# Optimization experiments

Measured on AMD Instinct MI355X. Metric: run time of the kernel, lower is better.

Reference implementation:

```python
import jax, jax.numpy as jnp
import numpy as np

N, E = 50000, 1600000
F_IN, F_EDGE, HID = 128, 16, 64
SLOPE = 0.2
EPS_BN = 1e-5


def setup_inputs() -> dict:
    key = jax.random.key(0)
    ks = jax.random.split(key, 24)
    g = lambda k, shp, s=0.1: (jax.random.normal(k, shp, dtype=jnp.float32) * s)
    inp = {
        'x': jax.random.normal(ks[0], (N, F_IN), dtype=jnp.float32),
        'edge_index': jax.random.randint(ks[1], (2, E), 0, N, dtype=jnp.int64),
        'edge_attr': jax.random.normal(ks[2], (E, F_EDGE), dtype=jnp.float32),
        # conv1: F_IN -> HID, 4 heads, concat
        'W1': g(ks[3], (F_IN, 4 * HID)), 'a1s': g(ks[4], (4, HID)), 'a1d': g(ks[5], (4, HID)), 'b1': jnp.zeros((4 * HID,), jnp.float32),
        # conv2: 4*HID -> HID, 4 heads, concat
        'W2': g(ks[6], (4 * HID, 4 * HID)), 'a2s': g(ks[7], (4, HID)), 'a2d': g(ks[8], (4, HID)), 'b2': jnp.zeros((4 * HID,), jnp.float32),
        # conv3: 4*HID -> HID, 1 head
        'W3': g(ks[9], (4 * HID, HID)), 'a3s': g(ks[10], (1, HID)), 'a3d': g(ks[11], (1, HID)), 'b3': jnp.zeros((HID,), jnp.float32),
        'bn1_g': jnp.ones((4 * HID,), jnp.float32), 'bn1_b': jnp.zeros((4 * HID,), jnp.float32),
        'bn2_g': jnp.ones((4 * HID,), jnp.float32), 'bn2_b': jnp.zeros((4 * HID,), jnp.float32),
        'mlp_W1': g(ks[12], (F_EDGE, HID)), 'mlp_b1': jnp.zeros((HID,), jnp.float32),
        'mlp_W2': g(ks[13], (HID, HID)), 'mlp_b2': jnp.zeros((HID,), jnp.float32),
        'fc_W': g(ks[14], (3 * HID, 1)), 'fc_b': jnp.zeros((1,), jnp.float32),
    }
    return inp


def _gat(x, W, a_s, a_d, b, src, dst, heads, dout):
    n = x.shape[0]
    h = (x @ W).reshape(n, heads, dout)                    # [N,H,D]
    ls = jnp.sum(h * a_s, axis=-1)                         # [N,H]
    ld = jnp.sum(h * a_d, axis=-1)
    logits = jax.nn.leaky_relu(ls[src] + ld[dst], SLOPE)   # [E',H]
    m = jax.ops.segment_max(logits, dst, num_segments=n)
    m = jnp.where(jnp.isfinite(m), m, 0.0)
    p = jnp.exp(logits - m[dst])
    s = jax.ops.segment_sum(p, dst, num_segments=n)
    alpha = p / (s[dst] + 1e-16)                           # segment softmax over in-edges
    out = jax.ops.segment_sum(h[src] * alpha[:, :, None], dst, num_segments=n)
    return out.reshape(n, heads * dout) + b


def _bn(x, g, b):
    mu = jnp.mean(x, axis=0)
    var = jnp.var(x, axis=0)
    return (x - mu) * jax.lax.rsqrt(var + EPS_BN) * g + b


def reference(x, edge_index, edge_attr, W1, a1s, a1d, b1, W2, a2s, a2d, b2,
              W3, a3s, a3d, b3, bn1_g, bn1_b, bn2_g, bn2_b,
              mlp_W1, mlp_b1, mlp_W2, mlp_b2, fc_W, fc_b):
    src0, dst0 = edge_index[0], edge_index[1]
    loop = jnp.arange(x.shape[0], dtype=edge_index.dtype)  # PyG adds self-loops
    src = jnp.concatenate([src0, loop])
    dst = jnp.concatenate([dst0, loop])

    h = _gat(x, W1, a1s, a1d, b1, src, dst, 4, HID)
    h = _bn(jax.nn.elu(h), bn1_g, bn1_b)
    h = _gat(h, W2, a2s, a2d, b2, src, dst, 4, HID)
    h = _bn(jax.nn.elu(h), bn2_g, bn2_b)
    h = _gat(h, W3, a3s, a3d, b3, src, dst, 1, HID)        # [N,HID]

    ef = jax.nn.relu(edge_attr @ mlp_W1 + mlp_b1) @ mlp_W2 + mlp_b2  # [E,HID]
    emb = jnp.concatenate([h[src0], h[dst0], ef], axis=1)  # [E,3*HID]
    return (emb @ fc_W + fc_b).squeeze(-1)
```

## Files before the change

kernel.cpp:

```cpp
#include <hip/hip_runtime.h>
#include <hip/hip_fp16.h>
#include <math.h>


#define FIN 128
#define HID 64
#define BIN_SHIFT 8

typedef _Float16 f16x8 __attribute__((ext_vector_type(8)));
typedef float f32x4 __attribute__((ext_vector_type(4)));

__device__ __forceinline__ unsigned short f2hbits(float f) {
    __half h = __float2half(f);
    return *reinterpret_cast<unsigned short*>(&h);
}
__device__ __forceinline__ float2 hpair(unsigned w) {
    __half2 h = *reinterpret_cast<__half2*>(&w);
    return __half22float2(h);
}

__device__ __forceinline__ unsigned fenc(float f) {
    unsigned b = __float_as_uint(f);
    return (b & 0x80000000u) ? ~b : (b | 0x80000000u);
}
__device__ __forceinline__ float fdec(unsigned k) {
    unsigned b = (k & 0x80000000u) ? (k ^ 0x80000000u) : ~k;
    return __uint_as_float(b);
}


__global__ __launch_bounds__(256) void bincount_kernel(const int* __restrict__ ei,
                                                       int* __restrict__ bincnt,
                                                       int E, int Etot) {
    __shared__ int h[256];
    int t = threadIdx.x;
    h[t] = 0;
    __syncthreads();
    int base = blockIdx.x * 4096;
    #pragma unroll
    for (int i = 0; i < 16; ++i) {
        int e = base + i * 256 + t;
        if (e < Etot) {
            int d = (e < E) ? ei[E + e] : (e - E);
            atomicAdd(&h[d >> BIN_SHIFT], 1);
        }
    }
    __syncthreads();
    if (h[t]) atomicAdd(&bincnt[t], h[t]);
}

__global__ void scanbins_kernel(const int* __restrict__ bincnt, int* __restrict__ binptr,
                                int* __restrict__ bincur, int NB, int Etot) {
    __shared__ int buf[256];
    int t = threadIdx.x;
    int v = (t < NB) ? bincnt[t] : 0;
    buf[t] = v;
    __syncthreads();
    for (int o = 1; o < 256; o <<= 1) {
        int y = (t >= o) ? buf[t - o] : 0;
        __syncthreads();
        buf[t] += y;
        __syncthreads();
    }
    int excl = buf[t] - v;
    if (t < NB) {
        binptr[t] = excl;
        bincur[t] = excl;
    }
    if (t == 0) binptr[NB] = Etot;
}

__global__ __launch_bounds__(256) void binscatter_kernel(const int* __restrict__ ei,
                                                         int* __restrict__ bincur,
                                                         int2* __restrict__ binned,
                                                         int E, int Etot) {
    __shared__ int h[256];
    __shared__ int gb[256];
    int t = threadIdx.x;
    h[t] = 0;
    __syncthreads();
    int base = blockIdx.x * 4096;
    #pragma unroll
    for (int i = 0; i < 16; ++i) {
        int e = base + i * 256 + t;
        if (e < Etot) {
            int d = (e < E) ? ei[E + e] : (e - E);
            atomicAdd(&h[d >> BIN_SHIFT], 1);
        }
    }
    __syncthreads();
    int cnt = h[t];
    if (cnt) gb[t] = atomicAdd(&bincur[t], cnt);
    __syncthreads();
    h[t] = 0;
    __syncthreads();
    #pragma unroll
    for (int i = 0; i < 16; ++i) {
        int e = base + i * 256 + t;
        if (e < Etot) {
            int s, d;
            if (e < E) { s = ei[e]; d = ei[E + e]; }
            else       { s = e - E; d = e - E; }
            int b = d >> BIN_SHIFT;
            int pos = gb[b] + atomicAdd(&h[b], 1);
            binned[pos] = make_int2(s, d);
        }
    }
}

__global__ __launch_bounds__(256) void bincsr_kernel(const int2* __restrict__ binned,
                                                     const int* __restrict__ binptr,
                                                     int* __restrict__ row_ptr,
                                                     int* __restrict__ col,
                                                     int N, int Etot) {
    __shared__ int h[256];
    __shared__ int cur[256];
    __shared__ int wsum[4];
    int b = blockIdx.x;
    int t = threadIdx.x;
    int lo = b << BIN_SHIFT;
    h[t] = 0;
    __syncthreads();
    int ebeg = binptr[b], eend = binptr[b + 1];
    for (int i = ebeg + t; i < eend; i += 256) atomicAdd(&h[binned[i].y - lo], 1);
    __syncthreads();
    int v = h[t];
    int lane = t & 63, w = t >> 6;
    int x = v;
    #pragma unroll
    for (int o = 1; o < 64; o <<= 1) {
        int y = __shfl_up(x, o);
        if (lane >= o) x += y;
    }
    if (lane == 63) wsum[w] = x;
    __syncthreads();
    int off = 0;
    #pragma unroll
    for (int i = 0; i < 4; ++i) off += (i < w) ? wsum[i] : 0;
    int excl = ebeg + off + x - v;
    int node = lo + t;
    if (node < N) row_ptr[node] = excl;
    cur[t] = excl;
    if (b == 0 && t == 0) row_ptr[N] = Etot;
    __syncthreads();
    for (int i = ebeg + t; i < eend; i += 256) {
        int2 sd = binned[i];
        int pos = atomicAdd(&cur[sd.y - lo], 1);
        col[pos] = sd.x;
    }
}


__global__ __launch_bounds__(256) void mfma_gemm_kernel(
    const float* __restrict__ X, const float* __restrict__ W,
    unsigned short* __restrict__ Yh, int Nrows, int K, int M,
    const float* __restrict__ bnsum, const float* __restrict__ bng,
    const float* __restrict__ bnb, float invN,
    const float* __restrict__ as_, const float* __restrict__ ad_,
    float* __restrict__ ls, float* __restrict__ ld,
    unsigned* __restrict__ lsmax_g, int slicedY) {
    __shared__ __align__(16) unsigned short a_lds[128][40];
    __shared__ __align__(16) unsigned short b_lds[64][40];
    __shared__ __align__(16) float scale_l[256];
    __shared__ __align__(16) float shift_l[256];
    __shared__ unsigned lmax_l;
    const int t = threadIdx.x;
    const int row0 = blockIdx.x * 128;
    const int by = blockIdx.y;
    const int c0 = by * 64;
    const int w = t >> 6, lane = t & 63;
    const int quad = lane >> 4, mrow = lane & 15;
    if (t == 0) lmax_l = 0;
    if (bnsum && t < 256) {
        float mu = bnsum[t] * invN;
        float var = bnsum[256 + t] * invN - mu * mu;
        float sc = bng[t] * rsqrtf(var + 1e-5f);
        scale_l[t] = sc;
        shift_l[t] = bnb[t] - mu * sc;
    }
    __syncthreads();
    f32x4 acc[2][4] = {};
    for (int k0 = 0; k0 < K; k0 += 32) {
        #pragma unroll
        for (int i = 0; i < 4; ++i) {
            int f = i * 256 + t;
            int r = f >> 3, kq = f & 7;
            int grow = row0 + r;
            float4 xv = make_float4(0.f, 0.f, 0.f, 0.f);
            if (grow < Nrows) xv = *(const float4*)(X + (size_t)grow * K + k0 + kq * 4);
            if (bnsum) {
                float4 sc = *(const float4*)&scale_l[k0 + kq * 4];
                float4 sh = *(const float4*)&shift_l[k0 + kq * 4];
                xv.x = fmaf(xv.x, sc.x, sh.x);
                xv.y = fmaf(xv.y, sc.y, sh.y);
                xv.z = fmaf(xv.z, sc.z, sh.z);
                xv.w = fmaf(xv.w, sc.w, sh.w);
            }
            ushort4 pk;
            pk.x = f2hbits(xv.x);
            pk.y = f2hbits(xv.y);
            pk.z = f2hbits(xv.z);
            pk.w = f2hbits(xv.w);
            *(ushort4*)&a_lds[r][kq * 4] = pk;
        }
        #pragma unroll
        for (int i = 0; i < 2; ++i) {
            int f = i * 256 + t;
            int kr = f >> 4, cq = f & 15;
            float4 wv = *(const float4*)(W + (size_t)(k0 + kr) * M + c0 + cq * 4);
            b_lds[cq * 4 + 0][kr] = f2hbits(wv.x);
            b_lds[cq * 4 + 1][kr] = f2hbits(wv.y);
            b_lds[cq * 4 + 2][kr] = f2hbits(wv.z);
            b_lds[cq * 4 + 3][kr] = f2hbits(wv.w);
        }
        __syncthreads();
        f16x8 a0 = *(const f16x8*)&a_lds[w * 32 + mrow][quad * 8];
        f16x8 a1 = *(const f16x8*)&a_lds[w * 32 + 16 + mrow][quad * 8];
        #pragma unroll
        for (int c = 0; c < 4; ++c) {
            f16x8 bf = *(const f16x8*)&b_lds[c * 16 + mrow][quad * 8];
            acc[0][c] = __builtin_amdgcn_mfma_f32_16x16x32_f16(a0, bf, acc[0][c], 0, 0, 0);
            acc[1][c] = __builtin_amdgcn_mfma_f32_16x16x32_f16(a1, bf, acc[1][c], 0, 0, 0);
        }
        __syncthreads();
    }
    #pragma unroll
    for (int i = 0; i < 2; ++i) {
        #pragma unroll
        for (int c = 0; c < 4; ++c) {
            #pragma unroll
            for (int r = 0; r < 4; ++r) {
                int grow = row0 + w * 32 + i * 16 + quad * 4 + r;
                if (grow < Nrows) {
                    int ch = c0 + c * 16 + mrow;
                    size_t idx = slicedY
                        ? ((size_t)(ch >> 5) * Nrows + grow) * 32 + (ch & 31)
                        : (size_t)grow * M + ch;
                    Yh[idx] = f2hbits(acc[i][c][r]);
                }
            }
        }
    }
    float asv[4], adv[4];
    #pragma unroll
    for (int c = 0; c < 4; ++c) {
        asv[c] = as_[by * 64 + c * 16 + mrow];
        adv[c] = ad_[by * 64 + c * 16 + mrow];
    }
    float lmax = -3.0e38f;
    #pragma unroll
    for (int i = 0; i < 2; ++i) {
        #pragma unroll
        for (int r = 0; r < 4; ++r) {
            float ps = 0.f, pd = 0.f;
            #pragma unroll
            for (int c = 0; c < 4; ++c) {
                ps = fmaf(acc[i][c][r], asv[c], ps);
                pd = fmaf(acc[i][c][r], adv[c], pd);
            }
            #pragma unroll
            for (int o = 1; o <= 8; o <<= 1) {
                ps += __shfl_xor(ps, o);
                pd += __shfl_xor(pd, o);
            }
            int grow = row0 + w * 32 + i * 16 + quad * 4 + r;
            if (mrow == 0 && grow < Nrows) {
                ls[(size_t)by * Nrows + grow] = ps;
                ld[(size_t)by * Nrows + grow] = pd;
                lmax = fmaxf(lmax, ps);
            }
        }
    }
    if (mrow == 0) atomicMax(&lmax_l, fenc(lmax));
    __syncthreads();
    if (t == 0) atomicMax(&lsmax_g[by], lmax_l);
}


#define ACC8(hv, p)                                              \
    {                                                            \
        float2 fa = hpair((hv).x), fb = hpair((hv).y);           \
        float2 fc = hpair((hv).z), fd = hpair((hv).w);           \
        a0 = fmaf((p), fa.x, a0); a1 = fmaf((p), fa.y, a1);      \
        a2 = fmaf((p), fb.x, a2); a3 = fmaf((p), fb.y, a3);      \
        a4 = fmaf((p), fc.x, a4); a5 = fmaf((p), fc.y, a5);      \
        a6 = fmaf((p), fd.x, a6); a7 = fmaf((p), fd.y, a7);      \
    }

#define COMPUTE_BATCH(l0_, l1_, l2_, l3_, h0_, h1_, h2_, h3_)    \
    {                                                            \
        float g0 = (l0_) + ldn_h; g0 = fmaxf(g0, 0.2f * g0);     \
        float g1 = (l1_) + ldn_h; g1 = fmaxf(g1, 0.2f * g1);     \
        float g2 = (l2_) + ldn_h; g2 = fmaxf(g2, 0.2f * g2);     \
        float g3 = (l3_) + ldn_h; g3 = fmaxf(g3, 0.2f * g3);     \
        float p0 = __expf(g0 - m_h), p1 = __expf(g1 - m_h);      \
        float p2 = __expf(g2 - m_h), p3 = __expf(g3 - m_h);      \
        psum += (p0 + p1) + (p2 + p3);                           \
        ACC8(h0_, p0) ACC8(h1_, p1) ACC8(h2_, p2) ACC8(h3_, p3)  \
    }

__global__ __launch_bounds__(256, 4) void agg_bn_kernel(
    const unsigned short* __restrict__ hb, const float* __restrict__ ls,
    const float* __restrict__ ld, const int* __restrict__ row_ptr,
    const int* __restrict__ col, const float* __restrict__ bias,
    const unsigned* __restrict__ lsmax_g, float* __restrict__ out,
    float* __restrict__ bnsum, int N) {
    __shared__ float redS[4][32];
    __shared__ float redQ[4][32];
    const int t = threadIdx.x;
    const int w = t >> 6, lane = t & 63;
    const int slice = blockIdx.x & 7;
    const int g = lane >> 2;
    const int c4 = lane & 3;
    const int hd = slice >> 1;
    const char* hsl = (const char*)hb + (size_t)slice * (size_t)N * 64u;
    const float* __restrict__ lsp = ls + (size_t)hd * N;
    const float* __restrict__ ldp = ld + (size_t)hd * N;
    const unsigned cb = (unsigned)c4 * 16u;
    const int cbase = slice * 32 + c4 * 8;
    const float lsm = fdec(lsmax_g[hd]);
    const float4 bvA = *(const float4*)(bias + cbase);
    const float4 bvB = *(const float4*)(bias + cbase + 4);
    const int sgid = (int)(blockIdx.x >> 3) * 64 + w * 16 + g;
    const int nsg = (int)(gridDim.x >> 3) * 64;
    float bns0 = 0.f, bns1 = 0.f, bns2 = 0.f, bns3 = 0.f;
    float bns4 = 0.f, bns5 = 0.f, bns6 = 0.f, bns7 = 0.f;
    float bnq0 = 0.f, bnq1 = 0.f, bnq2 = 0.f, bnq3 = 0.f;
    float bnq4 = 0.f, bnq5 = 0.f, bnq6 = 0.f, bnq7 = 0.f;
    for (int n = sgid; n < N; n += nsg) {
        int beg = row_ptr[n], end = row_ptr[n + 1];
        float ldn_h = ldp[n];
        float m_h = fmaxf(0.f, ldn_h + lsm);
        float psum = 0.f;
        float a0 = 0.f, a1 = 0.f, a2 = 0.f, a3 = 0.f;
        float a4 = 0.f, a5 = 0.f, a6 = 0.f, a7 = 0.f;
        int j = beg;
        const bool have = (j + 4 <= end);
        uint4 h0, h1, h2, h3;
        float l0 = 0.f, l1 = 0.f, l2 = 0.f, l3 = 0.f;
        if (have) {
            int s0 = col[j], s1 = col[j + 1], s2 = col[j + 2], s3 = col[j + 3];
            h0 = *(const uint4*)(hsl + ((unsigned)s0 * 64u + cb));
            h1 = *(const uint4*)(hsl + ((unsigned)s1 * 64u + cb));
            h2 = *(const uint4*)(hsl + ((unsigned)s2 * 64u + cb));
            h3 = *(const uint4*)(hsl + ((unsigned)s3 * 64u + cb));
            l0 = lsp[s0]; l1 = lsp[s1]; l2 = lsp[s2]; l3 = lsp[s3];
        }
        for (; j + 8 <= end; j += 4) {
            int n0 = col[j + 4], n1 = col[j + 5], n2 = col[j + 6], n3 = col[j + 7];
            uint4 q0 = *(const uint4*)(hsl + ((unsigned)n0 * 64u + cb));
            uint4 q1 = *(const uint4*)(hsl + ((unsigned)n1 * 64u + cb));
            uint4 q2 = *(const uint4*)(hsl + ((unsigned)n2 * 64u + cb));
            uint4 q3 = *(const uint4*)(hsl + ((unsigned)n3 * 64u + cb));
            float m0 = lsp[n0], m1 = lsp[n1], m2 = lsp[n2], m3 = lsp[n3];
            COMPUTE_BATCH(l0, l1, l2, l3, h0, h1, h2, h3)
            h0 = q0; h1 = q1; h2 = q2; h3 = q3;
            l0 = m0; l1 = m1; l2 = m2; l3 = m3;
        }
        if (have) {
            COMPUTE_BATCH(l0, l1, l2, l3, h0, h1, h2, h3)
            j += 4;
        }
        for (; j < end; ++j) {
            int s = col[j];
            uint4 hv = *(const uint4*)(hsl + ((unsigned)s * 64u + cb));
            float lv = lsp[s];
            float gg = lv + ldn_h; gg = fmaxf(gg, 0.2f * gg);
            float pv = __expf(gg - m_h);
            psum += pv;
            ACC8(hv, pv)
        }
        float inv = 1.f / (psum + 1e-16f);
        float o0 = fmaf(a0, inv, bvA.x);
        float o1 = fmaf(a1, inv, bvA.y);
        float o2 = fmaf(a2, inv, bvA.z);
        float o3 = fmaf(a3, inv, bvA.w);
        float o4 = fmaf(a4, inv, bvB.x);
        float o5 = fmaf(a5, inv, bvB.y);
        float o6 = fmaf(a6, inv, bvB.z);
        float o7 = fmaf(a7, inv, bvB.w);
        o0 = (o0 > 0.f) ? o0 : expm1f(o0);
        o1 = (o1 > 0.f) ? o1 : expm1f(o1);
        o2 = (o2 > 0.f) ? o2 : expm1f(o2);
        o3 = (o3 > 0.f) ? o3 : expm1f(o3);
        o4 = (o4 > 0.f) ? o4 : expm1f(o4);
        o5 = (o5 > 0.f) ? o5 : expm1f(o5);
        o6 = (o6 > 0.f) ? o6 : expm1f(o6);
        o7 = (o7 > 0.f) ? o7 : expm1f(o7);
        float* orow = out + (size_t)n * 256 + cbase;
        *(float4*)orow = make_float4(o0, o1, o2, o3);
        *(float4*)(orow + 4) = make_float4(o4, o5, o6, o7);
        bns0 += o0; bnq0 += o0 * o0;
        bns1 += o1; bnq1 += o1 * o1;
        bns2 += o2; bnq2 += o2 * o2;
        bns3 += o3; bnq3 += o3 * o3;
        bns4 += o4; bnq4 += o4 * o4;
        bns5 += o5; bnq5 += o5 * o5;
        bns6 += o6; bnq6 += o6 * o6;
        bns7 += o7; bnq7 += o7 * o7;
    }
    #pragma unroll
    for (int o = 4; o <= 32; o <<= 1) {
        bns0 += __shfl_xor(bns0, o); bnq0 += __shfl_xor(bnq0, o);
        bns1 += __shfl_xor(bns1, o); bnq1 += __shfl_xor(bnq1, o);
        bns2 += __shfl_xor(bns2, o); bnq2 += __shfl_xor(bnq2, o);
        bns3 += __shfl_xor(bns3, o); bnq3 += __shfl_xor(bnq3, o);
        bns4 += __shfl_xor(bns4, o); bnq4 += __shfl_xor(bnq4, o);
        bns5 += __shfl_xor(bns5, o); bnq5 += __shfl_xor(bnq5, o);
        bns6 += __shfl_xor(bns6, o); bnq6 += __shfl_xor(bnq6, o);
        bns7 += __shfl_xor(bns7, o); bnq7 += __shfl_xor(bnq7, o);
    }
    if (g == 0) {
        redS[w][c4 * 8 + 0] = bns0; redQ[w][c4 * 8 + 0] = bnq0;
        redS[w][c4 * 8 + 1] = bns1; redQ[w][c4 * 8 + 1] = bnq1;
        redS[w][c4 * 8 + 2] = bns2; redQ[w][c4 * 8 + 2] = bnq2;
        redS[w][c4 * 8 + 3] = bns3; redQ[w][c4 * 8 + 3] = bnq3;
        redS[w][c4 * 8 + 4] = bns4; redQ[w][c4 * 8 + 4] = bnq4;
        redS[w][c4 * 8 + 5] = bns5; redQ[w][c4 * 8 + 5] = bnq5;
        redS[w][c4 * 8 + 6] = bns6; redQ[w][c4 * 8 + 6] = bnq6;
        redS[w][c4 * 8 + 7] = bns7; redQ[w][c4 * 8 + 7] = bnq7;
    }
    __syncthreads();
    if (t < 32) {
        float s = redS[0][t] + redS[1][t] + redS[2][t] + redS[3][t];
        float q = redQ[0][t] + redQ[1][t] + redQ[2][t] + redQ[3][t];
        atomicAdd(&bnsum[slice * 32 + t], s);
        atomicAdd(&bnsum[256 + slice * 32 + t], q);
    }
}


__global__ __launch_bounds__(256) void agg3_kernel(
    const unsigned short* __restrict__ hb, const float* __restrict__ ls,
    const float* __restrict__ ld, const int* __restrict__ row_ptr,
    const int* __restrict__ col, const float* __restrict__ bias,
    const float* __restrict__ fcW, float* __restrict__ up, float* __restrict__ vp,
    const unsigned* __restrict__ lsmax_g, int N) {
    int lane = threadIdx.x & 63;
    int n = blockIdx.x * 4 + (threadIdx.x >> 6);
    if (n >= N) return;
    int beg = row_ptr[n], end = row_ptr[n + 1];
    float ldn = ld[n];
    float m_h = fmaxf(0.f, ldn + fdec(lsmax_g[0]));
    int g = lane >> 3;
    int li = lane & 7;
    int c0 = li * 8;
    const char* hbb = (const char*)hb;
    const unsigned cb = (unsigned)c0 * 2u;
    float psum = 0.f;
    float a0 = 0.f, a1 = 0.f, a2 = 0.f, a3 = 0.f;
    float a4 = 0.f, a5 = 0.f, a6 = 0.f, a7 = 0.f;
    for (int j = beg + g; j < end; j += 8) {
        int s = col[j];
        uint4 hv = *(const uint4*)(hbb + ((unsigned)s * 128u + cb));
        float lg = ls[s] + ldn;
        lg = fmaxf(lg, 0.2f * lg);
        float pv = __expf(lg - m_h);
        psum += pv;
        ACC8(hv, pv)
    }
    #pragma unroll
    for (int o = 8; o <= 32; o <<= 1) {
        psum += __shfl_xor(psum, o);
        a0 += __shfl_xor(a0, o); a1 += __shfl_xor(a1, o);
        a2 += __shfl_xor(a2, o); a3 += __shfl_xor(a3, o);
        a4 += __shfl_xor(a4, o); a5 += __shfl_xor(a5, o);
        a6 += __shfl_xor(a6, o); a7 += __shfl_xor(a7, o);
    }
    float inv = 1.f / (psum + 1e-16f);
    float v0 = fmaf(a0, inv, bias[c0 + 0]);
    float v1 = fmaf(a1, inv, bias[c0 + 1]);
    float v2 = fmaf(a2, inv, bias[c0 + 2]);
    float v3 = fmaf(a3, inv, bias[c0 + 3]);
    float v4 = fmaf(a4, inv, bias[c0 + 4]);
    float v5 = fmaf(a5, inv, bias[c0 + 5]);
    float v6 = fmaf(a6, inv, bias[c0 + 6]);
    float v7 = fmaf(a7, inv, bias[c0 + 7]);
    float pu = v0 * fcW[c0] + v1 * fcW[c0 + 1] + v2 * fcW[c0 + 2] + v3 * fcW[c0 + 3] +
               v4 * fcW[c0 + 4] + v5 * fcW[c0 + 5] + v6 * fcW[c0 + 6] + v7 * fcW[c0 + 7];
    float pv2 = v0 * fcW[64 + c0] + v1 * fcW[64 + c0 + 1] + v2 * fcW[64 + c0 + 2] +
                v3 * fcW[64 + c0 + 3] + v4 * fcW[64 + c0 + 4] + v5 * fcW[64 + c0 + 5] +
                v6 * fcW[64 + c0 + 6] + v7 * fcW[64 + c0 + 7];
    #pragma unroll
    for (int o = 1; o <= 4; o <<= 1) {
        pu += __shfl_xor(pu, o);
        pv2 += __shfl_xor(pv2, o);
    }
    if (lane == 0) {
        up[n] = pu;
        vp[n] = pv2;
    }
}


__global__ __launch_bounds__(256) void edge_out_kernel(
    const int* __restrict__ ei, const float* __restrict__ ea,
    const float* __restrict__ W1, const float* __restrict__ b1,
    const float* __restrict__ mlpW2, const float* __restrict__ mlpb2,
    const float* __restrict__ fcW, const float* __restrict__ fcb,
    const float* __restrict__ u, const float* __restrict__ v,
    float* __restrict__ out, int E) {
    __shared__ __align__(16) float W1T[64][16];
    __shared__ float w2fl[64];
    __shared__ float b1l[64];
    __shared__ float c2l;
    int t = threadIdx.x;
    for (int p = t; p < 1024; p += 256) {
        int i = p >> 6, j = p & 63;
        W1T[j][i] = W1[i * 64 + j];
    }
    if (t < 64) {
        float s = 0.f;
        for (int k = 0; k < 64; ++k) s = fmaf(mlpW2[t * 64 + k], fcW[128 + k], s);
        w2fl[t] = s;
        b1l[t] = b1[t];
    }
    if (t == 0) {
        float c = fcb[0];
        for (int k = 0; k < 64; ++k) c = fmaf(mlpb2[k], fcW[128 + k], c);
        c2l = c;
    }
    __syncthreads();
    int base = blockIdx.x * 1024;
    float eav[4][16];
    int sidx[4], didx[4];
    bool ok[4];
    #pragma unroll
    for (int k = 0; k < 4; ++k) {
        int e = base + k * 256 + t;
        ok[k] = e < E;
        int ec = ok[k] ? e : 0;
        sidx[k] = ei[ec];
        didx[k] = ei[E + ec];
        const float4* ear = (const float4*)(ea + (size_t)ec * 16);
        float4 q0 = ear[0], q1 = ear[1], q2 = ear[2], q3 = ear[3];
        eav[k][0] = q0.x;  eav[k][1] = q0.y;  eav[k][2] = q0.z;  eav[k][3] = q0.w;
        eav[k][4] = q1.x;  eav[k][5] = q1.y;  eav[k][6] = q1.z;  eav[k][7] = q1.w;
        eav[k][8] = q2.x;  eav[k][9] = q2.y;  eav[k][10] = q2.z; eav[k][11] = q2.w;
        eav[k][12] = q3.x; eav[k][13] = q3.y; eav[k][14] = q3.z; eav[k][15] = q3.w;
    }
    float acc[4] = {0.f, 0.f, 0.f, 0.f};
    #pragma unroll 4
    for (int j = 0; j < 64; ++j) {
        const float4* wr = (const float4*)&W1T[j][0];
        float4 w0 = wr[0], w1 = wr[1], w2 = wr[2], w3 = wr[3];
        float wrow[16] = {w0.x, w0.y, w0.z, w0.w, w1.x, w1.y, w1.z, w1.w,
                          w2.x, w2.y, w2.z, w2.w, w3.x, w3.y, w3.z, w3.w};
        float bj = b1l[j], wj = w2fl[j];
        #pragma unroll
        for (int k = 0; k < 4; ++k) {
            float s = bj;
            #pragma unroll
            for (int q = 0; q < 16; ++q) s = fmaf(eav[k][q], wrow[q], s);
            s = fmaxf(s, 0.f);
            acc[k] = fmaf(s, wj, acc[k]);
        }
    }
    float cc = c2l;
    #pragma unroll
    for (int k = 0; k < 4; ++k) {
        if (ok[k]) {
            int e = base + k * 256 + t;
            out[e] = u[sidx[k]] + v[didx[k]] + acc[k] + cc;
        }
    }
}


extern "C" void kernel_launch(void* const* d_in, const int* in_sizes, int n_in,
                              void* d_out, int out_size, void* d_ws, size_t ws_size,
                              hipStream_t stream) {
    const float* x     = (const float*)d_in[0];
    const int*   ei    = (const int*)d_in[1];
    const float* ea    = (const float*)d_in[2];
    const float* W1    = (const float*)d_in[3];
    const float* a1s   = (const float*)d_in[4];
    const float* a1d   = (const float*)d_in[5];
    const float* b1    = (const float*)d_in[6];
    const float* W2    = (const float*)d_in[7];
    const float* a2s   = (const float*)d_in[8];
    const float* a2d   = (const float*)d_in[9];
    const float* b2    = (const float*)d_in[10];
    const float* W3    = (const float*)d_in[11];
    const float* a3s   = (const float*)d_in[12];
    const float* a3d   = (const float*)d_in[13];
    const float* b3    = (const float*)d_in[14];
    const float* bn1g  = (const float*)d_in[15];
    const float* bn1b  = (const float*)d_in[16];
    const float* bn2g  = (const float*)d_in[17];
    const float* bn2b  = (const float*)d_in[18];
    const float* mlpW1 = (const float*)d_in[19];
    const float* mlpb1 = (const float*)d_in[20];
    const float* mlpW2 = (const float*)d_in[21];
    const float* mlpb2 = (const float*)d_in[22];
    const float* fcW   = (const float*)d_in[23];
    const float* fcb   = (const float*)d_in[24];
    float* out = (float*)d_out;

    const int N = in_sizes[0] / FIN;
    const int E = in_sizes[1] / 2;
    const int Etot = E + N;
    const int NB = (N + 255) >> BIN_SHIFT;

    char* wsb = (char*)d_ws;
    size_t off = 0;
    auto alloc = [&](size_t bytes) {
        void* p = wsb + off;
        off += (bytes + 63) & ~(size_t)63;
        return p;
    };
    unsigned short* hAb = (unsigned short*)alloc((size_t)N * 256 * 2);
    float* hB  = (float*)alloc((size_t)N * 256 * 4);
    unsigned short* h3b = (unsigned short*)alloc((size_t)N * 64 * 2);
    float* lsb = (float*)alloc((size_t)N * 4 * 4);
    float* ldb = (float*)alloc((size_t)N * 4 * 4);
    int* row_ptr = (int*)alloc((size_t)(N + 1) * 4);
    int* colb    = (int*)alloc((size_t)Etot * 4);
    int2* binned = (int2*)alloc((size_t)Etot * 8);
    int* zreg    = (int*)alloc((256 + 16 + 512 + 512) * 4);
    int* bincnt  = zreg;
    unsigned* lsmax1 = (unsigned*)(zreg + 256);
    unsigned* lsmax2 = lsmax1 + 4;
    unsigned* lsmax3 = lsmax1 + 8;
    float* bnsumA = (float*)(zreg + 256 + 16);
    float* bnsumB = bnsumA + 512;
    int* binptr  = (int*)alloc((size_t)(NB + 1) * 4);
    int* bincur  = (int*)alloc((size_t)NB * 4);
    float* ub  = (float*)alloc((size_t)N * 4);
    float* vb  = (float*)alloc((size_t)N * 4);
    (void)ws_size; (void)n_in; (void)out_size;

    const int nb4 = (N + 3) / 4;
    const int nch = (Etot + 4095) / 4096;
    const float invN = 1.f / (float)N;

    hipMemsetAsync(zreg, 0, (256 + 16 + 512 + 512) * sizeof(int), stream);
    bincount_kernel<<<nch, 256, 0, stream>>>(ei, bincnt, E, Etot);
    scanbins_kernel<<<1, 256, 0, stream>>>(bincnt, binptr, bincur, NB, Etot);
    binscatter_kernel<<<nch, 256, 0, stream>>>(ei, bincur, binned, E, Etot);
    bincsr_kernel<<<NB, 256, 0, stream>>>(binned, binptr, row_ptr, colb, N, Etot);

    dim3 ggrid((N + 127) / 128, 4);
    dim3 ggrid3((N + 127) / 128, 1);

    mfma_gemm_kernel<<<ggrid, 256, 0, stream>>>(x, W1, hAb, N, 128, 256,
        nullptr, nullptr, nullptr, invN, a1s, a1d, lsb, ldb, lsmax1, 1);
    agg_bn_kernel<<<1024, 256, 0, stream>>>(hAb, lsb, ldb, row_ptr, colb, b1,
                                            lsmax1, hB, bnsumA, N);
    mfma_gemm_kernel<<<ggrid, 256, 0, stream>>>(hB, W2, hAb, N, 256, 256,
        bnsumA, bn1g, bn1b, invN, a2s, a2d, lsb, ldb, lsmax2, 1);
    agg_bn_kernel<<<1024, 256, 0, stream>>>(hAb, lsb, ldb, row_ptr, colb, b2,
                                            lsmax2, hB, bnsumB, N);
    mfma_gemm_kernel<<<ggrid3, 256, 0, stream>>>(hB, W3, h3b, N, 256, 64,
        bnsumB, bn2g, bn2b, invN, a3s, a3d, lsb, ldb, lsmax3, 0);
    agg3_kernel<<<nb4, 256, 0, stream>>>(h3b, lsb, ldb, row_ptr, colb, b3,
                                         fcW, ub, vb, lsmax3, N);
    edge_out_kernel<<<(E + 1023) / 1024, 256, 0, stream>>>(
        ei, ea, mlpW1, mlpb1, mlpW2, mlpb2, fcW, fcb, ub, vb, out, E);
}
```

Baseline: 775.2 us.

## Bind aggregation feature slices to XCDs with atomic work-stealing cursors

The aggregation kernel reads the hardware XCD id and makes each wave start on the feature slice matching its XCD, rotating through all eight slices. Nodes are handed out in chunks of 16 by per-slice atomic cursors instead of a fixed grid stride. The goal is to keep each slice's gathered rows in one XCD's L2 and to balance uneven in-degree work, with occupancy raised to 8 blocks and the grid doubled. In exchange it adds per-wave atomics on the cursors, more atomics on the BN statistics (one set per wave per slice instead of per block), and depends on an undocumented hardware register layout.

Result: slower. 2.638 ms (+240.3%).

```diff
diff --git a/kernel.cpp b/kernel.cpp
--- a/kernel.cpp
+++ b/kernel.cpp
@@ -26,6 +26,11 @@
 __device__ __forceinline__ float fdec(unsigned k) {
     unsigned b = (k & 0x80000000u) ? (k ^ 0x80000000u) : ~k;
     return __uint_as_float(b);
+}
+
+#define HWREG_ENC(id, off, sz) ((id) | ((off) << 6) | (((sz) - 1) << 11))
+__device__ __forceinline__ unsigned get_xcd() {
+    return __builtin_amdgcn_s_getreg(HWREG_ENC(20, 0, 32)) & 7u;
 }
 
 
@@ -299,133 +304,137 @@
         ACC8(h0_, p0) ACC8(h1_, p1) ACC8(h2_, p2) ACC8(h3_, p3)  \
     }
 
-__global__ __launch_bounds__(256, 4) void agg_bn_kernel(
+__global__ __launch_bounds__(256, 8) void agg_bn_kernel(
     const unsigned short* __restrict__ hb, const float* __restrict__ ls,
     const float* __restrict__ ld, const int* __restrict__ row_ptr,
     const int* __restrict__ col, const float* __restrict__ bias,
     const unsigned* __restrict__ lsmax_g, float* __restrict__ out,
-    float* __restrict__ bnsum, int N) {
-    __shared__ float redS[4][32];
-    __shared__ float redQ[4][32];
-    const int t = threadIdx.x;
-    const int w = t >> 6, lane = t & 63;
-    const int slice = blockIdx.x & 7;
+    float* __restrict__ bnsum, int* __restrict__ cursor, int N) {
+    const int lane = threadIdx.x & 63;
     const int g = lane >> 2;
     const int c4 = lane & 3;
-    const int hd = slice >> 1;
-    const char* hsl = (const char*)hb + (size_t)slice * (size_t)N * 64u;
-    const float* __restrict__ lsp = ls + (size_t)hd * N;
-    const float* __restrict__ ldp = ld + (size_t)hd * N;
-    const unsigned cb = (unsigned)c4 * 16u;
-    const int cbase = slice * 32 + c4 * 8;
-    const float lsm = fdec(lsmax_g[hd]);
-    const float4 bvA = *(const float4*)(bias + cbase);
-    const float4 bvB = *(const float4*)(bias + cbase + 4);
-    const int sgid = (int)(blockIdx.x >> 3) * 64 + w * 16 + g;
-    const int nsg = (int)(gridDim.x >> 3) * 64;
-    float bns0 = 0.f, bns1 = 0.f, bns2 = 0.f, bns3 = 0.f;
-    float bns4 = 0.f, bns5 = 0.f, bns6 = 0.f, bns7 = 0.f;
-    float bnq0 = 0.f, bnq1 = 0.f, bnq2 = 0.f, bnq3 = 0.f;
-    float bnq4 = 0.f, bnq5 = 0.f, bnq6 = 0.f, bnq7 = 0.f;
-    for (int n = sgid; n < N; n += nsg) {
-        int beg = row_ptr[n], end = row_ptr[n + 1];
-        float ldn_h = ldp[n];
-        float m_h = fmaxf(0.f, ldn_h + lsm);
-        float psum = 0.f;
-        float a0 = 0.f, a1 = 0.f, a2 = 0.f, a3 = 0.f;
-        float a4 = 0.f, a5 = 0.f, a6 = 0.f, a7 = 0.f;
-        int j = beg;
-        const bool have = (j + 4 <= end);
-        uint4 h0, h1, h2, h3;
-        float l0 = 0.f, l1 = 0.f, l2 = 0.f, l3 = 0.f;
-        if (have) {
-            int s0 = col[j], s1 = col[j + 1], s2 = col[j + 2], s3 = col[j + 3];
-            h0 = *(const uint4*)(hsl + ((unsigned)s0 * 64u + cb));
-            h1 = *(const uint4*)(hsl + ((unsigned)s1 * 64u + cb));
-            h2 = *(const uint4*)(hsl + ((unsigned)s2 * 64u + cb));
-            h3 = *(const uint4*)(hsl + ((unsigned)s3 * 64u + cb));
-            l0 = lsp[s0]; l1 = lsp[s1]; l2 = lsp[s2]; l3 = lsp[s3];
-        }
-        for (; j + 8 <= end; j += 4) {
-            int n0 = col[j + 4], n1 = col[j + 5], n2 = col[j + 6], n3 = col[j + 7];
-            uint4 q0 = *(const uint4*)(hsl + ((unsigned)n0 * 64u + cb));
-            uint4 q1 = *(const uint4*)(hsl + ((unsigned)n1 * 64u + cb));
-            uint4 q2 = *(const uint4*)(hsl + ((unsigned)n2 * 64u + cb));
-            uint4 q3 = *(const uint4*)(hsl + ((unsigned)n3 * 64u + cb));
-            float m0 = lsp[n0], m1 = lsp[n1], m2 = lsp[n2], m3 = lsp[n3];
-            COMPUTE_BATCH(l0, l1, l2, l3, h0, h1, h2, h3)
-            h0 = q0; h1 = q1; h2 = q2; h3 = q3;
-            l0 = m0; l1 = m1; l2 = m2; l3 = m3;
-        }
-        if (have) {
-            COMPUTE_BATCH(l0, l1, l2, l3, h0, h1, h2, h3)
-            j += 4;
-        }
-        for (; j < end; ++j) {
-            int s = col[j];
-            uint4 hv = *(const uint4*)(hsl + ((unsigned)s * 64u + cb));
-            float lv = lsp[s];
-            float gg = lv + ldn_h; gg = fmaxf(gg, 0.2f * gg);
-            float pv = __expf(gg - m_h);
-            psum += pv;
-            ACC8(hv, pv)
-        }
-        float inv = 1.f / (psum + 1e-16f);
-        float o0 = fmaf(a0, inv, bvA.x);
-        float o1 = fmaf(a1, inv, bvA.y);
-        float o2 = fmaf(a2, inv, bvA.z);
-        float o3 = fmaf(a3, inv, bvA.w);
-        float o4 = fmaf(a4, inv, bvB.x);
-        float o5 = fmaf(a5, inv, bvB.y);
-        float o6 = fmaf(a6, inv, bvB.z);
-        float o7 = fmaf(a7, inv, bvB.w);
-        o0 = (o0 > 0.f) ? o0 : expm1f(o0);
-        o1 = (o1 > 0.f) ? o1 : expm1f(o1);
-        o2 = (o2 > 0.f) ? o2 : expm1f(o2);
-        o3 = (o3 > 0.f) ? o3 : expm1f(o3);
-        o4 = (o4 > 0.f) ? o4 : expm1f(o4);
-        o5 = (o5 > 0.f) ? o5 : expm1f(o5);
-        o6 = (o6 > 0.f) ? o6 : expm1f(o6);
-        o7 = (o7 > 0.f) ? o7 : expm1f(o7);
-        float* orow = out + (size_t)n * 256 + cbase;
-        *(float4*)orow = make_float4(o0, o1, o2, o3);
-        *(float4*)(orow + 4) = make_float4(o4, o5, o6, o7);
-        bns0 += o0; bnq0 += o0 * o0;
-        bns1 += o1; bnq1 += o1 * o1;
-        bns2 += o2; bnq2 += o2 * o2;
-        bns3 += o3; bnq3 += o3 * o3;
-        bns4 += o4; bnq4 += o4 * o4;
-        bns5 += o5; bnq5 += o5 * o5;
-        bns6 += o6; bnq6 += o6 * o6;
-        bns7 += o7; bnq7 += o7 * o7;
-    }
-    #pragma unroll
-    for (int o = 4; o <= 32; o <<= 1) {
-        bns0 += __shfl_xor(bns0, o); bnq0 += __shfl_xor(bnq0, o);
-        bns1 += __shfl_xor(bns1, o); bnq1 += __shfl_xor(bnq1, o);
-        bns2 += __shfl_xor(bns2, o); bnq2 += __shfl_xor(bnq2, o);
-        bns3 += __shfl_xor(bns3, o); bnq3 += __shfl_xor(bnq3, o);
-        bns4 += __shfl_xor(bns4, o); bnq4 += __shfl_xor(bnq4, o);
-        bns5 += __shfl_xor(bns5, o); bnq5 += __shfl_xor(bnq5, o);
-        bns6 += __shfl_xor(bns6, o); bnq6 += __shfl_xor(bnq6, o);
-        bns7 += __shfl_xor(bns7, o); bnq7 += __shfl_xor(bnq7, o);
-    }
-    if (g == 0) {
-        redS[w][c4 * 8 + 0] = bns0; redQ[w][c4 * 8 + 0] = bnq0;
-        redS[w][c4 * 8 + 1] = bns1; redQ[w][c4 * 8 + 1] = bnq1;
-        redS[w][c4 * 8 + 2] = bns2; redQ[w][c4 * 8 + 2] = bnq2;
-        redS[w][c4 * 8 + 3] = bns3; redQ[w][c4 * 8 + 3] = bnq3;
-        redS[w][c4 * 8 + 4] = bns4; redQ[w][c4 * 8 + 4] = bnq4;
-        redS[w][c4 * 8 + 5] = bns5; redQ[w][c4 * 8 + 5] = bnq5;
-        redS[w][c4 * 8 + 6] = bns6; redQ[w][c4 * 8 + 6] = bnq6;
-        redS[w][c4 * 8 + 7] = bns7; redQ[w][c4 * 8 + 7] = bnq7;
-    }
-    __syncthreads();
-    if (t < 32) {
-        float s = redS[0][t] + redS[1][t] + redS[2][t] + redS[3][t];
-        float q = redQ[0][t] + redQ[1][t] + redQ[2][t] + redQ[3][t];
-        atomicAdd(&bnsum[slice * 32 + t], s);
-        atomicAdd(&bnsum[256 + slice * 32 + t], q);
+    const unsigned xcd = get_xcd();
+    for (int ss = 0; ss < 8; ++ss) {
+        const int sl = (int)((xcd + ss) & 7u);
+        const int hd = sl >> 1;
+        const char* hsl = (const char*)hb + (size_t)sl * (size_t)N * 64u;
+        const float* __restrict__ lsp = ls + (size_t)hd * N;
+        const float* __restrict__ ldp = ld + (size_t)hd * N;
+        const unsigned cb = (unsigned)c4 * 16u;
+        const int cbase = sl * 32 + c4 * 8;
+        const float lsm = fdec(lsmax_g[hd]);
+        const float4 bvA = *(const float4*)(bias + cbase);
+        const float4 bvB = *(const float4*)(bias + cbase + 4);
+        float bns0 = 0.f, bns1 = 0.f, bns2 = 0.f, bns3 = 0.f;
+        float bns4 = 0.f, bns5 = 0.f, bns6 = 0.f, bns7 = 0.f;
+        float bnq0 = 0.f, bnq1 = 0.f, bnq2 = 0.f, bnq3 = 0.f;
+        float bnq4 = 0.f, bnq5 = 0.f, bnq6 = 0.f, bnq7 = 0.f;
+        bool did = false;
+        for (;;) {
+            int base = 0;
+            if (lane == 0) base = atomicAdd(&cursor[sl], 16);
+            base = __shfl(base, 0);
+            if (base >= N) break;
+            did = true;
+            int n = base + g;
+            if (n < N) {
+                int beg = row_ptr[n], end = row_ptr[n + 1];
+                float ldn_h = ldp[n];
+                float m_h = fmaxf(0.f, ldn_h + lsm);
+                float psum = 0.f;
+                float a0 = 0.f, a1 = 0.f, a2 = 0.f, a3 = 0.f;
+                float a4 = 0.f, a5 = 0.f, a6 = 0.f, a7 = 0.f;
+                int j = beg;
+                const bool have = (j + 4 <= end);
+                uint4 h0, h1, h2, h3;
+                float l0 = 0.f, l1 = 0.f, l2 = 0.f, l3 = 0.f;
+                if (have) {
+                    int s0 = col[j], s1 = col[j + 1], s2 = col[j + 2], s3 = col[j + 3];
+                    h0 = *(const uint4*)(hsl + ((unsigned)s0 * 64u + cb));
+                    h1 = *(const uint4*)(hsl + ((unsigned)s1 * 64u + cb));
+                    h2 = *(const uint4*)(hsl + ((unsigned)s2 * 64u + cb));
+                    h3 = *(const uint4*)(hsl + ((unsigned)s3 * 64u + cb));
+                    l0 = lsp[s0]; l1 = lsp[s1]; l2 = lsp[s2]; l3 = lsp[s3];
+                }
+                for (; j + 8 <= end; j += 4) {
+                    int n0 = col[j + 4], n1 = col[j + 5], n2 = col[j + 6], n3 = col[j + 7];
+                    uint4 q0 = *(const uint4*)(hsl + ((unsigned)n0 * 64u + cb));
+                    uint4 q1 = *(const uint4*)(hsl + ((unsigned)n1 * 64u + cb));
+                    uint4 q2 = *(const uint4*)(hsl + ((unsigned)n2 * 64u + cb));
+                    uint4 q3 = *(const uint4*)(hsl + ((unsigned)n3 * 64u + cb));
+                    float m0 = lsp[n0], m1 = lsp[n1], m2 = lsp[n2], m3 = lsp[n3];
+                    COMPUTE_BATCH(l0, l1, l2, l3, h0, h1, h2, h3)
+                    h0 = q0; h1 = q1; h2 = q2; h3 = q3;
+                    l0 = m0; l1 = m1; l2 = m2; l3 = m3;
+                }
+                if (have) {
+                    COMPUTE_BATCH(l0, l1, l2, l3, h0, h1, h2, h3)
+                    j += 4;
+                }
+                for (; j < end; ++j) {
+                    int s = col[j];
+                    uint4 hv = *(const uint4*)(hsl + ((unsigned)s * 64u + cb));
+                    float lv = lsp[s];
+                    float gg = lv + ldn_h; gg = fmaxf(gg, 0.2f * gg);
+                    float pv = __expf(gg - m_h);
+                    psum += pv;
+                    ACC8(hv, pv)
+                }
+                float inv = 1.f / (psum + 1e-16f);
+                float o0 = fmaf(a0, inv, bvA.x);
+                float o1 = fmaf(a1, inv, bvA.y);
+                float o2 = fmaf(a2, inv, bvA.z);
+                float o3 = fmaf(a3, inv, bvA.w);
+                float o4 = fmaf(a4, inv, bvB.x);
+                float o5 = fmaf(a5, inv, bvB.y);
+                float o6 = fmaf(a6, inv, bvB.z);
+                float o7 = fmaf(a7, inv, bvB.w);
+                o0 = (o0 > 0.f) ? o0 : expm1f(o0);
+                o1 = (o1 > 0.f) ? o1 : expm1f(o1);
+                o2 = (o2 > 0.f) ? o2 : expm1f(o2);
+                o3 = (o3 > 0.f) ? o3 : expm1f(o3);
+                o4 = (o4 > 0.f) ? o4 : expm1f(o4);
+                o5 = (o5 > 0.f) ? o5 : expm1f(o5);
+                o6 = (o6 > 0.f) ? o6 : expm1f(o6);
+                o7 = (o7 > 0.f) ? o7 : expm1f(o7);
+                float* orow = out + (size_t)n * 256 + cbase;
+                *(float4*)orow = make_float4(o0, o1, o2, o3);
+                *(float4*)(orow + 4) = make_float4(o4, o5, o6, o7);
+                bns0 += o0; bnq0 += o0 * o0;
+                bns1 += o1; bnq1 += o1 * o1;
+                bns2 += o2; bnq2 += o2 * o2;
+                bns3 += o3; bnq3 += o3 * o3;
+                bns4 += o4; bnq4 += o4 * o4;
+                bns5 += o5; bnq5 += o5 * o5;
+                bns6 += o6; bnq6 += o6 * o6;
+                bns7 += o7; bnq7 += o7 * o7;
+            }
+        }
+        if (did) {
+            #pragma unroll
+            for (int o = 4; o <= 32; o <<= 1) {
+                bns0 += __shfl_xor(bns0, o); bnq0 += __shfl_xor(bnq0, o);
+                bns1 += __shfl_xor(bns1, o); bnq1 += __shfl_xor(bnq1, o);
+                bns2 += __shfl_xor(bns2, o); bnq2 += __shfl_xor(bnq2, o);
+                bns3 += __shfl_xor(bns3, o); bnq3 += __shfl_xor(bnq3, o);
+                bns4 += __shfl_xor(bns4, o); bnq4 += __shfl_xor(bnq4, o);
+                bns5 += __shfl_xor(bns5, o); bnq5 += __shfl_xor(bnq5, o);
+                bns6 += __shfl_xor(bns6, o); bnq6 += __shfl_xor(bnq6, o);
+                bns7 += __shfl_xor(bns7, o); bnq7 += __shfl_xor(bnq7, o);
+            }
+            if (lane < 4) {
+                float* bs = bnsum + cbase;
+                float* bq = bnsum + 256 + cbase;
+                atomicAdd(bs + 0, bns0); atomicAdd(bq + 0, bnq0);
+                atomicAdd(bs + 1, bns1); atomicAdd(bq + 1, bnq1);
+                atomicAdd(bs + 2, bns2); atomicAdd(bq + 2, bnq2);
+                atomicAdd(bs + 3, bns3); atomicAdd(bq + 3, bnq3);
+                atomicAdd(bs + 4, bns4); atomicAdd(bq + 4, bnq4);
+                atomicAdd(bs + 5, bns5); atomicAdd(bq + 5, bnq5);
+                atomicAdd(bs + 6, bns6); atomicAdd(bq + 6, bnq6);
+                atomicAdd(bs + 7, bns7); atomicAdd(bq + 7, bnq7);
+            }
+        }
     }
 }
 
@@ -617,13 +626,15 @@
     int* row_ptr = (int*)alloc((size_t)(N + 1) * 4);
     int* colb    = (int*)alloc((size_t)Etot * 4);
     int2* binned = (int2*)alloc((size_t)Etot * 8);
-    int* zreg    = (int*)alloc((256 + 16 + 512 + 512) * 4);
+    int* zreg    = (int*)alloc((256 + 16 + 512 + 512 + 16) * 4);
     int* bincnt  = zreg;
     unsigned* lsmax1 = (unsigned*)(zreg + 256);
     unsigned* lsmax2 = lsmax1 + 4;
     unsigned* lsmax3 = lsmax1 + 8;
     float* bnsumA = (float*)(zreg + 256 + 16);
     float* bnsumB = bnsumA + 512;
+    int* cursorA = zreg + 256 + 16 + 1024;
+    int* cursorB = cursorA + 8;
     int* binptr  = (int*)alloc((size_t)(NB + 1) * 4);
     int* bincur  = (int*)alloc((size_t)NB * 4);
     float* ub  = (float*)alloc((size_t)N * 4);
@@ -634,7 +645,7 @@
     const int nch = (Etot + 4095) / 4096;
     const float invN = 1.f / (float)N;
 
-    hipMemsetAsync(zreg, 0, (256 + 16 + 512 + 512) * sizeof(int), stream);
+    hipMemsetAsync(zreg, 0, (256 + 16 + 512 + 512 + 16) * sizeof(int), stream);
     bincount_kernel<<<nch, 256, 0, stream>>>(ei, bincnt, E, Etot);
     scanbins_kernel<<<1, 256, 0, stream>>>(bincnt, binptr, bincur, NB, Etot);
     binscatter_kernel<<<nch, 256, 0, stream>>>(ei, bincur, binned, E, Etot);
@@ -645,12 +656,12 @@
 
     mfma_gemm_kernel<<<ggrid, 256, 0, stream>>>(x, W1, hAb, N, 128, 256,
         nullptr, nullptr, nullptr, invN, a1s, a1d, lsb, ldb, lsmax1, 1);
-    agg_bn_kernel<<<1024, 256, 0, stream>>>(hAb, lsb, ldb, row_ptr, colb, b1,
-                                            lsmax1, hB, bnsumA, N);
+    agg_bn_kernel<<<2048, 256, 0, stream>>>(hAb, lsb, ldb, row_ptr, colb, b1,
+                                            lsmax1, hB, bnsumA, cursorA, N);
     mfma_gemm_kernel<<<ggrid, 256, 0, stream>>>(hB, W2, hAb, N, 256, 256,
         bnsumA, bn1g, bn1b, invN, a2s, a2d, lsb, ldb, lsmax2, 1);
-    agg_bn_kernel<<<1024, 256, 0, stream>>>(hAb, lsb, ldb, row_ptr, colb, b2,
-                                            lsmax2, hB, bnsumB, N);
+    agg_bn_kernel<<<2048, 256, 0, stream>>>(hAb, lsb, ldb, row_ptr, colb, b2,
+                                            lsmax2, hB, bnsumB, cursorB, N);
     mfma_gemm_kernel<<<ggrid3, 256, 0, stream>>>(hB, W3, h3b, N, 256, 64,
         bnsumB, bn2g, bn2b, invN, a3s, a3d, lsb, ldb, lsmax3, 0);
     agg3_kernel<<<nb4, 256, 0, stream>>>(h3b, lsb, ldb, row_ptr, colb, b3,
```
